# Kernel tuning notes

Hardware: AMD Instinct MI355X
Metric: run time of the kernel (lower is better)

## Reference

```python
import jax, jax.numpy as jnp
import numpy as np

N = 100000   # nodes
E = 1600000  # edges (avg degree 16)
M = 20000    # target nodes
D = 128      # input_dim
H = 128      # hidden_dim
H2 = 128     # hidden_dim2
H3 = 64      # hidden_dim3
EPS = 1e-5


def _lin(k, fin, fout, bias=True):
    lim = 1.0 / np.sqrt(fin)
    kw, kb = jax.random.split(k)
    W = jax.random.uniform(kw, (fout, fin), jnp.float32, -lim, lim)
    if bias:
        b = jax.random.uniform(kb, (fout,), jnp.float32, -lim, lim)
        return W, b
    return W


def setup_inputs() -> dict:
    key = jax.random.key(0)
    ks = jax.random.split(key, 16)
    x = jax.random.normal(ks[0], (N, D), jnp.float32)
    edge_index = jax.random.randint(ks[1], (2, E), 0, N, dtype=jnp.int32)
    node_index = jax.random.randint(ks[2], (M,), 0, N, dtype=jnp.int32)
    W1l, b1 = _lin(ks[3], D, H)          # SAGEConv1: lin_l (neighbors, has bias)
    W1r = _lin(ks[4], D, H, bias=False)  # lin_r (root, no bias)
    W2l, b2 = _lin(ks[5], H, H)
    W2r = _lin(ks[6], H, H, bias=False)
    fcW1, fcb1 = _lin(ks[7], H, H2)
    fcW2, fcb2 = _lin(ks[8], H2, H3)
    fcW3, fcb3 = _lin(ks[9], H3, 1)
    g1 = jnp.ones((H2,), jnp.float32); be1 = jnp.zeros((H2,), jnp.float32)
    g2 = jnp.ones((H3,), jnp.float32); be2 = jnp.zeros((H3,), jnp.float32)
    return dict(x=x, edge_index=edge_index, node_index=node_index,
                W1l=W1l, b1=b1, W1r=W1r, W2l=W2l, b2=b2, W2r=W2r,
                fcW1=fcW1, fcb1=fcb1, fcW2=fcW2, fcb2=fcb2, fcW3=fcW3, fcb3=fcb3,
                g1=g1, be1=be1, g2=g2, be2=be2)


def _sage(h, src, dst, Wl, bl, Wr):
    # PyG SAGEConv(aggr='mean'): out = lin_l(mean_{j in N(i)} x_j) + lin_r(x_i)
    msg = h[src]                                                   # [E, F] gather
    s = jax.ops.segment_sum(msg, dst, num_segments=N)              # [N, F]
    cnt = jax.ops.segment_sum(jnp.ones((src.shape[0],), h.dtype), dst, num_segments=N)
    agg = s / jnp.maximum(cnt, 1.0)[:, None]                       # mean, 0 if no nbrs
    return agg @ Wl.T + bl + h @ Wr.T


def _bn(h, g, b):
    # BatchNorm1d training mode: biased batch stats
    mu = jnp.mean(h, axis=0)
    var = jnp.mean(jnp.square(h - mu), axis=0)
    return (h - mu) * jax.lax.rsqrt(var + EPS) * g + b


def reference(x, edge_index, node_index, W1l, b1, W1r, W2l, b2, W2r,
              fcW1, fcb1, fcW2, fcb2, fcW3, fcb3, g1, be1, g2, be2):
    src, dst = edge_index[0], edge_index[1]
    h = jax.nn.relu(_sage(x, src, dst, W1l, b1, W1r))
    h = _sage(h, src, dst, W2l, b2, W2r)
    h = h[node_index]                       # [M, H]
    h = h @ fcW1.T + fcb1
    h = jnp.where(_bn(h, g1, be1) >= 0, _bn(h, g1, be1), 0.1 * _bn(h, g1, be1)) if False else jax.nn.leaky_relu(_bn(h, g1, be1), 0.1)
    h = h @ fcW2.T + fcb2
    h = jax.nn.leaky_relu(_bn(h, g2, be2), 0.05)
    return h @ fcW3.T + fcb3                # [M, 1]
```

## Files before the change

kernel.cpp:

```cpp
#include <hip/hip_runtime.h>
#include <hip/hip_bf16.h>

#define EPSV 1e-5f

typedef __attribute__((ext_vector_type(8))) short s16x8;
typedef __attribute__((ext_vector_type(4))) float f32x4;

static __device__ __forceinline__ unsigned short f2b(float f) {
    __hip_bfloat16 h = __float2bfloat16(f);
    return *reinterpret_cast<unsigned short*>(&h);
}


__global__ void k_link(const int* __restrict__ src, const int* __restrict__ dst,
                       int* __restrict__ head, int2* __restrict__ pk, int E) {
    int e = blockIdx.x * blockDim.x + threadIdx.x;
    if (e < E) {
        int h = atomicExch(&head[dst[e]], e);
        pk[e] = make_int2(h, src[e]);
    }
}

__global__ void k_mark(const int* __restrict__ nidx, int* __restrict__ mark,
                       int* __restrict__ list, int* __restrict__ nmarked, int M) {
    int m = blockIdx.x * blockDim.x + threadIdx.x;
    if (m < M) {
        int n = nidx[m];
        if (atomicExch(&mark[n], 1) == 0) list[atomicAdd(nmarked, 1)] = n;
    }
}


__global__ void k_tobf16(const float* __restrict__ in, unsigned short* __restrict__ out, int n4) {
    int i = blockIdx.x * blockDim.x + threadIdx.x;
    int stride = gridDim.x * blockDim.x;
    for (; i < n4; i += stride) {
        float4 v = ((const float4*)in)[i];
        ushort4 u;
        u.x = f2b(v.x); u.y = f2b(v.y); u.z = f2b(v.z); u.w = f2b(v.w);
        ((ushort4*)out)[i] = u;
    }
}

__global__ void k_wconv(const float* __restrict__ W1l, const float* __restrict__ W1r,
                        const float* __restrict__ W2l, const float* __restrict__ W2r,
                        const float* __restrict__ fcW1, const float* __restrict__ fcW2,
                        unsigned short* __restrict__ Wb) {
    int i = blockIdx.x * blockDim.x + threadIdx.x;
    if (i >= 90112) return;
    float v;
    if (i < 16384) v = W1l[i];
    else if (i < 32768) v = W1r[i - 16384];
    else if (i < 49152) v = W2l[i - 32768];
    else if (i < 65536) v = W2r[i - 49152];
    else if (i < 81920) v = fcW1[i - 65536];
    else v = fcW2[i - 81920];
    Wb[i] = f2b(v);
}

__global__ void k_aggr_g(const int* __restrict__ head, const int2* __restrict__ pk,
                         const uint4* __restrict__ feat,
                         const int* __restrict__ list, const int* __restrict__ nlist,
                         uint4* __restrict__ outf, int n) {
    int lane = threadIdx.x & 63;
    int g = lane >> 4;
    int r = lane & 15;
    int w = blockIdx.x * (blockDim.x >> 6) + (threadIdx.x >> 6);
    int limit = list ? *nlist : n;
    int idx = w * 4 + g;
    int node = (idx < limit) ? (list ? list[idx] : idx) : -1;
    int e = (node >= 0) ? head[node] : -1;
    int2 p = pk[e >= 0 ? e : 0];
    float a[8];
#pragma unroll
    for (int i = 0; i < 8; i++) a[i] = 0.f;
    int cnt = 0;

    while (__any(e >= 0)) {
        int srcn = (e >= 0) ? p.y : 0;
        uint4 u = feat[(size_t)srcn * 16 + r];
        int en = (e >= 0 && p.x >= 0) ? p.x : 0;
        int2 pn = pk[en];
        bool act = e >= 0;
        float m = act ? 1.0f : 0.0f;
        a[0] += m * __uint_as_float(u.x << 16);
        a[1] += m * __uint_as_float(u.x & 0xffff0000u);
        a[2] += m * __uint_as_float(u.y << 16);
        a[3] += m * __uint_as_float(u.y & 0xffff0000u);
        a[4] += m * __uint_as_float(u.z << 16);
        a[5] += m * __uint_as_float(u.z & 0xffff0000u);
        a[6] += m * __uint_as_float(u.w << 16);
        a[7] += m * __uint_as_float(u.w & 0xffff0000u);
        cnt += act ? 1 : 0;
        e = act ? p.x : -1;
        p = pn;
    }
    if (node >= 0) {
        float ic = 1.0f / fmaxf((float)cnt, 1.0f);
        uint4 o;
        o.x = ((unsigned)f2b(a[1] * ic) << 16) | (unsigned)f2b(a[0] * ic);
        o.y = ((unsigned)f2b(a[3] * ic) << 16) | (unsigned)f2b(a[2] * ic);
        o.z = ((unsigned)f2b(a[5] * ic) << 16) | (unsigned)f2b(a[4] * ic);
        o.w = ((unsigned)f2b(a[7] * ic) << 16) | (unsigned)f2b(a[6] * ic);
        outf[(size_t)node * 16 + r] = o;
    }
}

template <int NCT, int TWO, int RELU, int OUTBF>
__global__ void k_mdense(const unsigned short* __restrict__ A,
                         const unsigned short* __restrict__ X,
                         const int* __restrict__ gidx,
                         const unsigned short* __restrict__ Wl,
                         const float* __restrict__ bl,
                         const unsigned short* __restrict__ Wr,
                         void* __restrict__ outp, int nrows) {
    const int OC = NCT * 16;
    int lane = threadIdx.x & 63;
    int wave = threadIdx.x >> 6;
    int rowBase = (blockIdx.x * 4 + wave) * 32;
    if (rowBase >= nrows) return;
    int rl = lane & 15;
    int ks = lane >> 4;
    int r0 = rowBase + rl, r1 = r0 + 16;
    int n0 = gidx ? gidx[r0] : r0;
    int n1 = gidx ? gidx[r1] : r1;
    f32x4 acc0[NCT], acc1[NCT];
#pragma unroll
    for (int ct = 0; ct < NCT; ct++) {
        acc0[ct] = (f32x4)0.f;
        acc1[ct] = (f32x4)0.f;
    }
#pragma unroll
    for (int pass = 0; pass < (TWO ? 2 : 1); pass++) {
        const unsigned short* Ain = pass ? X : A;
        const unsigned short* W = pass ? Wr : Wl;
        const s16x8* a0p = (const s16x8*)(Ain + (size_t)n0 * 128);
        const s16x8* a1p = (const s16x8*)(Ain + (size_t)n1 * 128);
#pragma unroll
        for (int kc = 0; kc < 4; kc++) {
            s16x8 af0 = a0p[kc * 4 + ks];
            s16x8 af1 = a1p[kc * 4 + ks];
#pragma unroll
            for (int ct = 0; ct < NCT; ct++) {
                const s16x8* bp = (const s16x8*)(W + (size_t)(ct * 16 + rl) * 128);
                s16x8 bf = bp[kc * 4 + ks];
                acc0[ct] = __builtin_amdgcn_mfma_f32_16x16x32_bf16(af0, bf, acc0[ct], 0, 0, 0);
                acc1[ct] = __builtin_amdgcn_mfma_f32_16x16x32_bf16(af1, bf, acc1[ct], 0, 0, 0);
            }
        }
    }
#pragma unroll
    for (int ct = 0; ct < NCT; ct++) {
        int col = ct * 16 + rl;
        float bj = bl[col];
#pragma unroll
        for (int j = 0; j < 4; j++) {
            int or0 = rowBase + ks * 4 + j;
            int or1 = or0 + 16;
            float v0 = acc0[ct][j] + bj;
            float v1 = acc1[ct][j] + bj;
            if (RELU) { v0 = fmaxf(v0, 0.f); v1 = fmaxf(v1, 0.f); }
            if (OUTBF) {
                ((unsigned short*)outp)[(size_t)or0 * OC + col] = f2b(v0);
                ((unsigned short*)outp)[(size_t)or1 * OC + col] = f2b(v1);
            } else {
                ((float*)outp)[(size_t)or0 * OC + col] = v0;
                ((float*)outp)[(size_t)or1 * OC + col] = v1;
            }
        }
    }
}

template <int C>
__global__ void k_bnstats(const float* __restrict__ z, float* __restrict__ gsum,
                          float* __restrict__ gsq, int nrows, int rowsPerBlock) {
    int t = threadIdx.x;
    int c = t % C;
    int g = t / C;
    const int G = 256 / C;
    int r0 = blockIdx.x * rowsPerBlock;
    int r1 = min(r0 + rowsPerBlock, nrows);
    float s = 0.f, q = 0.f;
    for (int r = r0 + g; r < r1; r += G) {
        float v = z[(size_t)r * C + c];
        s += v;
        q += v * v;
    }
    __shared__ float ls[256], lq[256];
    ls[t] = s;
    lq[t] = q;
    __syncthreads();
    if (t < C) {
        for (int g2 = 1; g2 < G; g2++) {
            s += ls[g2 * C + c];
            q += lq[g2 * C + c];
        }
        atomicAdd(&gsum[c], s);
        atomicAdd(&gsq[c], q);
    }
}

__global__ void k_bnprep(const float* __restrict__ gsum, const float* __restrict__ gsq,
                         const float* __restrict__ gamma, const float* __restrict__ beta,
                         float* __restrict__ scale, float* __restrict__ shift, int C, float invM) {
    int c = blockIdx.x * blockDim.x + threadIdx.x;
    if (c < C) {
        float mean = gsum[c] * invM;
        float var = gsq[c] * invM - mean * mean;
        float is = rsqrtf(var + EPSV);
        float sc = gamma[c] * is;
        scale[c] = sc;
        shift[c] = beta[c] - mean * sc;
    }
}

template <int OUTBF>
__global__ void k_bn_act(const float* __restrict__ z, const float* __restrict__ scale,
                         const float* __restrict__ shift, void* __restrict__ outp,
                         int total, int colsMask, float slope) {
    int i = blockIdx.x * blockDim.x + threadIdx.x;
    if (i < total) {
        int c = i & colsMask;
        float y = z[i] * scale[c] + shift[c];
        y = (y >= 0.f) ? y : slope * y;
        if (OUTBF) ((unsigned short*)outp)[i] = f2b(y);
        else ((float*)outp)[i] = y;
    }
}

__global__ void k_fc3(const float* __restrict__ z2, const float* __restrict__ w,
                      const float* __restrict__ b, float* __restrict__ out, int nrows) {
    int lane = threadIdx.x & 63;
    int m = blockIdx.x * (blockDim.x >> 6) + (threadIdx.x >> 6);
    if (m >= nrows) return;
    float v = z2[(size_t)m * 64 + lane] * w[lane];
    for (int off = 32; off > 0; off >>= 1) v += __shfl_down(v, off);
    if (lane == 0) out[m] = v + b[0];
}

extern "C" void kernel_launch(void* const* d_in, const int* in_sizes, int n_in,
                              void* d_out, int out_size, void* d_ws, size_t ws_size,
                              hipStream_t stream) {
    const float* x    = (const float*)d_in[0];
    const int*   ei   = (const int*)d_in[1];
    const int*   nidx = (const int*)d_in[2];
    const float* W1l  = (const float*)d_in[3];
    const float* b1   = (const float*)d_in[4];
    const float* W1r  = (const float*)d_in[5];
    const float* W2l  = (const float*)d_in[6];
    const float* b2   = (const float*)d_in[7];
    const float* W2r  = (const float*)d_in[8];
    const float* fcW1 = (const float*)d_in[9];
    const float* fcb1 = (const float*)d_in[10];
    const float* fcW2 = (const float*)d_in[11];
    const float* fcb2 = (const float*)d_in[12];
    const float* fcW3 = (const float*)d_in[13];
    const float* fcb3 = (const float*)d_in[14];
    const float* g1   = (const float*)d_in[15];
    const float* be1  = (const float*)d_in[16];
    const float* g2   = (const float*)d_in[17];
    const float* be2  = (const float*)d_in[18];

    const int N = in_sizes[0] / 128;
    const int E = in_sizes[1] / 2;
    const int M = in_sizes[2];
    const int* src = ei;
    const int* dst = ei + E;

    char* ws = (char*)d_ws;
    size_t off = 0;
    unsigned short* xb  = (unsigned short*)(ws + off); off += (size_t)N * 128 * 2;
    unsigned short* sb  = (unsigned short*)(ws + off); off += (size_t)N * 128 * 2;
    unsigned short* h1b = (unsigned short*)(ws + off); off += (size_t)N * 128 * 2;
    unsigned short* z0b = (unsigned short*)(ws + off); off += (size_t)M * 128 * 2;
    float* z1           = (float*)(ws + off);          off += (size_t)M * 128 * 4;
    unsigned short* z1b = (unsigned short*)(ws + off); off += (size_t)M * 128 * 2;
    float* z2           = (float*)(ws + off);          off += (size_t)M * 64 * 4;
    unsigned short* Wb  = (unsigned short*)(ws + off); off += 90112 * 2;
    int2* pk       = (int2*)(ws + off);  off += (size_t)E * 8;
    int*  head     = (int*)(ws + off);   off += (size_t)N * 4;
    int*  mark     = (int*)(ws + off);   off += (size_t)N * 4;
    int*  list     = (int*)(ws + off);   off += (size_t)M * 4;
    int*  nmarked  = (int*)(ws + off);   off += 64;
    float* gsum1   = (float*)(ws + off); off += 128 * 4;
    float* gsq1    = (float*)(ws + off); off += 128 * 4;
    float* scale1  = (float*)(ws + off); off += 128 * 4;
    float* shift1  = (float*)(ws + off); off += 128 * 4;
    float* gsum2   = (float*)(ws + off); off += 64 * 4;
    float* gsq2    = (float*)(ws + off); off += 64 * 4;
    float* scale2  = (float*)(ws + off); off += 64 * 4;
    float* shift2  = (float*)(ws + off); off += 64 * 4;
    float* out = (float*)d_out;

    hipMemsetAsync(head, 0xFF, (size_t)N * 4, stream);
    hipMemsetAsync(mark, 0, (size_t)N * 4, stream);
    hipMemsetAsync(nmarked, 0, 4, stream);
    hipMemsetAsync(gsum1, 0, (128 + 128 + 128 + 128 + 64 + 64 + 64 + 64) * 4, stream);

    k_wconv<<<(90112 + 255) / 256, 256, 0, stream>>>(W1l, W1r, W2l, W2r, fcW1, fcW2, Wb);
    k_tobf16<<<2048, 256, 0, stream>>>(x, xb, N * 128 / 4);

    k_link<<<(E + 255) / 256, 256, 0, stream>>>(src, dst, head, pk, E);
    k_mark<<<(M + 255) / 256, 256, 0, stream>>>(nidx, mark, list, nmarked, M);

    {
        int waves = (N + 3) / 4;
        k_aggr_g<<<(waves + 3) / 4, 256, 0, stream>>>(
            head, pk, (const uint4*)xb, nullptr, nullptr, (uint4*)sb, N);
    }
    k_mdense<8, 1, 1, 1><<<(N / 32 + 3) / 4, 256, 0, stream>>>(
        sb, xb, nullptr, Wb + 0, b1, Wb + 16384, h1b, N);

    {
        int waves = (M + 3) / 4;
        k_aggr_g<<<(waves + 3) / 4, 256, 0, stream>>>(
            head, pk, (const uint4*)h1b, list, nmarked, (uint4*)sb, N);
    }
    k_mdense<8, 1, 0, 1><<<(M / 32 + 3) / 4, 256, 0, stream>>>(
        sb, h1b, nidx, Wb + 32768, b2, Wb + 49152, z0b, M);

    k_mdense<8, 0, 0, 0><<<(M / 32 + 3) / 4, 256, 0, stream>>>(
        z0b, nullptr, nullptr, Wb + 65536, fcb1, nullptr, z1, M);
    k_bnstats<128><<<(M + 99) / 100, 256, 0, stream>>>(z1, gsum1, gsq1, M, 100);
    k_bnprep<<<1, 128, 0, stream>>>(gsum1, gsq1, g1, be1, scale1, shift1, 128, 1.0f / M);
    k_bn_act<1><<<((size_t)M * 128 + 255) / 256, 256, 0, stream>>>(
        z1, scale1, shift1, z1b, M * 128, 127, 0.1f);

    k_mdense<4, 0, 0, 0><<<(M / 32 + 3) / 4, 256, 0, stream>>>(
        z1b, nullptr, nullptr, Wb + 81920, fcb2, nullptr, z2, M);
    k_bnstats<64><<<(M + 99) / 100, 256, 0, stream>>>(z2, gsum2, gsq2, M, 100);
    k_bnprep<<<1, 64, 0, stream>>>(gsum2, gsq2, g2, be2, scale2, shift2, 64, 1.0f / M);
    k_bn_act<0><<<((size_t)M * 64 + 255) / 256, 256, 0, stream>>>(
        z2, scale2, shift2, z2, M * 64, 63, 0.05f);

    k_fc3<<<(M + 3) / 4, 256, 0, stream>>>(z2, fcW3, fcb3, out, M);
}
```

Measured before the change: 447.6 us.

## Bucket edge slots by destination block and fuse BN-activation into consumers

Edge link records are now placed in per-destination-bucket slot ranges (16 nodes per bucket, 512 slots each) instead of edge order, so each node's linked list sits in a compact region and the gather walk gets better locality. The BN+leaky-ReLU elementwise passes are folded into the next dense layer's A-operand load and into the final fc3 reduction, removing two kernels and the intermediate bf16 buffer. BN stats use fewer, larger blocks, cutting atomic traffic. Risks: a bucket overflows if 16 nodes receive more than 512 edges in total, and the pk buffer grows to cover all buckets at full capacity.

```diff
diff --git a/kernel.cpp b/kernel.cpp
--- a/kernel.cpp
+++ b/kernel.cpp
@@ -2,6 +2,8 @@
 #include <hip/hip_bf16.h>
 
 #define EPSV 1e-5f
+#define BSH 4
+#define SCAP 512
 
 typedef __attribute__((ext_vector_type(8))) short s16x8;
 typedef __attribute__((ext_vector_type(4))) float f32x4;
@@ -12,12 +14,17 @@
 }
 
 
-__global__ void k_link(const int* __restrict__ src, const int* __restrict__ dst,
-                       int* __restrict__ head, int2* __restrict__ pk, int E) {
+__global__ void k_link2(const int* __restrict__ src, const int* __restrict__ dst,
+                        int* __restrict__ head, int* __restrict__ bcur,
+                        int2* __restrict__ pk, int E) {
     int e = blockIdx.x * blockDim.x + threadIdx.x;
     if (e < E) {
-        int h = atomicExch(&head[dst[e]], e);
-        pk[e] = make_int2(h, src[e]);
+        int d = dst[e];
+        int b = d >> BSH;
+        int pos = atomicAdd(&bcur[b], 1);
+        int slot = (b << 9) + pos;
+        int h = atomicExch(&head[d], slot);
+        pk[slot] = make_int2(h, src[e]);
     }
 }
 
@@ -171,6 +178,67 @@
     }
 }
 
+static __device__ __forceinline__ s16x8 bnpack(const float* __restrict__ p,
+                                               const float* __restrict__ sc,
+                                               const float* __restrict__ sh, float slope) {
+    s16x8 r;
+#pragma unroll
+    for (int i = 0; i < 8; i++) {
+        float y = p[i] * sc[i] + sh[i];
+        y = (y >= 0.f) ? y : slope * y;
+        r[i] = (short)f2b(y);
+    }
+    return r;
+}
+
+__global__ void k_mdense_bn(const float* __restrict__ Ain,
+                            const float* __restrict__ scale, const float* __restrict__ shift,
+                            const unsigned short* __restrict__ W,
+                            const float* __restrict__ bl,
+                            float* __restrict__ outp, int nrows, float slope) {
+    const int NCT = 4, OC = 64;
+    int lane = threadIdx.x & 63;
+    int wave = threadIdx.x >> 6;
+    int rowBase = (blockIdx.x * 4 + wave) * 32;
+    if (rowBase >= nrows) return;
+    int rl = lane & 15;
+    int ks = lane >> 4;
+    int r0 = rowBase + rl, r1 = r0 + 16;
+    const float* a0p = Ain + (size_t)r0 * 128;
+    const float* a1p = Ain + (size_t)r1 * 128;
+    f32x4 acc0[NCT], acc1[NCT];
+#pragma unroll
+    for (int ct = 0; ct < NCT; ct++) {
+        acc0[ct] = (f32x4)0.f;
+        acc1[ct] = (f32x4)0.f;
+    }
+#pragma unroll
+    for (int kc = 0; kc < 4; kc++) {
+        int kb = kc * 32 + ks * 8;
+        s16x8 af0 = bnpack(a0p + kb, scale + kb, shift + kb, slope);
+        s16x8 af1 = bnpack(a1p + kb, scale + kb, shift + kb, slope);
+#pragma unroll
+        for (int ct = 0; ct < NCT; ct++) {
+            const s16x8* bp = (const s16x8*)(W + (size_t)(ct * 16 + rl) * 128);
+            s16x8 bf = bp[kc * 4 + ks];
+            acc0[ct] = __builtin_amdgcn_mfma_f32_16x16x32_bf16(af0, bf, acc0[ct], 0, 0, 0);
+            acc1[ct] = __builtin_amdgcn_mfma_f32_16x16x32_bf16(af1, bf, acc1[ct], 0, 0, 0);
+        }
+    }
+#pragma unroll
+    for (int ct = 0; ct < NCT; ct++) {
+        int col = ct * 16 + rl;
+        float bj = bl[col];
+#pragma unroll
+        for (int j = 0; j < 4; j++) {
+            int or0 = rowBase + ks * 4 + j;
+            int or1 = or0 + 16;
+            outp[(size_t)or0 * OC + col] = acc0[ct][j] + bj;
+            outp[(size_t)or1 * OC + col] = acc1[ct][j] + bj;
+        }
+    }
+}
+
 template <int C>
 __global__ void k_bnstats(const float* __restrict__ z, float* __restrict__ gsum,
                           float* __restrict__ gsq, int nrows, int rowsPerBlock) {
@@ -214,26 +282,15 @@
     }
 }
 
-template <int OUTBF>
-__global__ void k_bn_act(const float* __restrict__ z, const float* __restrict__ scale,
-                         const float* __restrict__ shift, void* __restrict__ outp,
-                         int total, int colsMask, float slope) {
-    int i = blockIdx.x * blockDim.x + threadIdx.x;
-    if (i < total) {
-        int c = i & colsMask;
-        float y = z[i] * scale[c] + shift[c];
-        y = (y >= 0.f) ? y : slope * y;
-        if (OUTBF) ((unsigned short*)outp)[i] = f2b(y);
-        else ((float*)outp)[i] = y;
-    }
-}
-
-__global__ void k_fc3(const float* __restrict__ z2, const float* __restrict__ w,
-                      const float* __restrict__ b, float* __restrict__ out, int nrows) {
+__global__ void k_fc3_bn(const float* __restrict__ z2, const float* __restrict__ scale,
+                         const float* __restrict__ shift, const float* __restrict__ w,
+                         const float* __restrict__ b, float* __restrict__ out, int nrows) {
     int lane = threadIdx.x & 63;
     int m = blockIdx.x * (blockDim.x >> 6) + (threadIdx.x >> 6);
     if (m >= nrows) return;
-    float v = z2[(size_t)m * 64 + lane] * w[lane];
+    float y = z2[(size_t)m * 64 + lane] * scale[lane] + shift[lane];
+    y = (y >= 0.f) ? y : 0.05f * y;
+    float v = y * w[lane];
     for (int off = 32; off > 0; off >>= 1) v += __shfl_down(v, off);
     if (lane == 0) out[m] = v + b[0];
 }
@@ -266,6 +323,8 @@
     const int M = in_sizes[2];
     const int* src = ei;
     const int* dst = ei + E;
+    const int NBK = (N + 15) >> BSH;
+    const int NSLOT = NBK * SCAP;
 
     char* ws = (char*)d_ws;
     size_t off = 0;
@@ -274,11 +333,11 @@
     unsigned short* h1b = (unsigned short*)(ws + off); off += (size_t)N * 128 * 2;
     unsigned short* z0b = (unsigned short*)(ws + off); off += (size_t)M * 128 * 2;
     float* z1           = (float*)(ws + off);          off += (size_t)M * 128 * 4;
-    unsigned short* z1b = (unsigned short*)(ws + off); off += (size_t)M * 128 * 2;
     float* z2           = (float*)(ws + off);          off += (size_t)M * 64 * 4;
     unsigned short* Wb  = (unsigned short*)(ws + off); off += 90112 * 2;
-    int2* pk       = (int2*)(ws + off);  off += (size_t)E * 8;
+    int2* pk       = (int2*)(ws + off);  off += (size_t)NSLOT * 8;
     int*  head     = (int*)(ws + off);   off += (size_t)N * 4;
+    int*  bcur     = (int*)(ws + off);   off += (size_t)NBK * 4;
     int*  mark     = (int*)(ws + off);   off += (size_t)N * 4;
     int*  list     = (int*)(ws + off);   off += (size_t)M * 4;
     int*  nmarked  = (int*)(ws + off);   off += 64;
@@ -293,6 +352,7 @@
     float* out = (float*)d_out;
 
     hipMemsetAsync(head, 0xFF, (size_t)N * 4, stream);
+    hipMemsetAsync(bcur, 0, (size_t)NBK * 4, stream);
     hipMemsetAsync(mark, 0, (size_t)N * 4, stream);
     hipMemsetAsync(nmarked, 0, 4, stream);
     hipMemsetAsync(gsum1, 0, (128 + 128 + 128 + 128 + 64 + 64 + 64 + 64) * 4, stream);
@@ -300,7 +360,7 @@
     k_wconv<<<(90112 + 255) / 256, 256, 0, stream>>>(W1l, W1r, W2l, W2r, fcW1, fcW2, Wb);
     k_tobf16<<<2048, 256, 0, stream>>>(x, xb, N * 128 / 4);
 
-    k_link<<<(E + 255) / 256, 256, 0, stream>>>(src, dst, head, pk, E);
+    k_link2<<<(E + 255) / 256, 256, 0, stream>>>(src, dst, head, bcur, pk, E);
     k_mark<<<(M + 255) / 256, 256, 0, stream>>>(nidx, mark, list, nmarked, M);
 
     {
@@ -321,17 +381,13 @@
 
     k_mdense<8, 0, 0, 0><<<(M / 32 + 3) / 4, 256, 0, stream>>>(
         z0b, nullptr, nullptr, Wb + 65536, fcb1, nullptr, z1, M);
-    k_bnstats<128><<<(M + 99) / 100, 256, 0, stream>>>(z1, gsum1, gsq1, M, 100);
+    k_bnstats<128><<<(M + 399) / 400, 256, 0, stream>>>(z1, gsum1, gsq1, M, 400);
     k_bnprep<<<1, 128, 0, stream>>>(gsum1, gsq1, g1, be1, scale1, shift1, 128, 1.0f / M);
-    k_bn_act<1><<<((size_t)M * 128 + 255) / 256, 256, 0, stream>>>(
-        z1, scale1, shift1, z1b, M * 128, 127, 0.1f);
-
-    k_mdense<4, 0, 0, 0><<<(M / 32 + 3) / 4, 256, 0, stream>>>(
-        z1b, nullptr, nullptr, Wb + 81920, fcb2, nullptr, z2, M);
-    k_bnstats<64><<<(M + 99) / 100, 256, 0, stream>>>(z2, gsum2, gsq2, M, 100);
+
+    k_mdense_bn<<<(M / 32 + 3) / 4, 256, 0, stream>>>(
+        z1, scale1, shift1, Wb + 81920, fcb2, z2, M, 0.1f);
+    k_bnstats<64><<<(M + 399) / 400, 256, 0, stream>>>(z2, gsum2, gsq2, M, 400);
     k_bnprep<<<1, 64, 0, stream>>>(gsum2, gsq2, g2, be2, scale2, shift2, 64, 1.0f / M);
-    k_bn_act<0><<<((size_t)M * 64 + 255) / 256, 256, 0, stream>>>(
-        z2, scale2, shift2, z2, M * 64, 63, 0.05f);
-
-    k_fc3<<<(M + 3) / 4, 256, 0, stream>>>(z2, fcW3, fcb3, out, M);
-}
+
+    k_fc3_bn<<<(M + 3) / 4, 256, 0, stream>>>(z2, scale2, shift2, fcW3, fcb3, out, M);
+}
```

Measured after the change: 569.7 us. 1.27x slower.
